# Kernel tuning notes

Hardware: AMD Instinct MI355X
Metric: run time of the kernel (lower is better)

Reference implementation:

```python
import jax, jax.numpy as jnp
import numpy as np

B, T, C, H, W = 32, 128, 64, 8, 8
NF = 64
CIN = C * H * W           # 4096
GOUT = NF * H * W         # 4096


def setup_inputs() -> dict:
    key = jax.random.key(0)
    ks = jax.random.split(key, 9)
    s_in = 1.0 / np.sqrt(CIN)
    return {
        "input1": jax.random.normal(ks[0], (B, T, C, H, W), jnp.float32),
        "input2": jax.random.normal(ks[1], (B, T, C, H, W), jnp.float32),
        "act_weights": jax.random.uniform(ks[2], (3,), jnp.float32),
        "w1": jax.random.normal(ks[3], (NF, CIN), jnp.float32) * s_in,
        "b1": jax.random.normal(ks[4], (NF,), jnp.float32) * s_in,
        "w2": jax.random.normal(ks[5], (NF, CIN), jnp.float32) * s_in,
        "b2": jax.random.normal(ks[6], (NF,), jnp.float32) * s_in,
        "wg": jax.random.normal(ks[7], (GOUT, CIN), jnp.float32) * s_in,
        "bg": jax.random.normal(ks[8], (GOUT,), jnp.float32) * s_in,
    }


def reference(input1, input2, act_weights, w1, b1, w2, b2, wg, bg):
    # flatten spatial+channel dims: [B, T, CIN]
    x1 = input1.reshape(B, T, CIN)
    x2 = input2.reshape(B, T, CIN)
    # 1x1 Conv1d == per-timestep linear projection (computed ONCE, unlike torch src)
    q = jnp.einsum("btc,fc->btf", x1, w1) + b1          # [B, T, NF]
    k = jnp.einsum("btc,fc->btf", x2, w2) + b2          # [B, T, NF]
    g = jnp.einsum("btc,gc->btg", x1, wg) + bg          # [B, T, GOUT]
    # QK^T: conv1(x1)^T @ conv2(x2) -> [B, T, T]
    scores = jnp.einsum("btf,bsf->bts", q, k)
    # three activation branches fused via weighted sum; softmax dim=1 (over first T axis)
    act = (act_weights[0] * jax.nn.relu(scores)
           + act_weights[1] * jax.nn.sigmoid(scores)
           + act_weights[2] * jax.nn.softmax(scores, axis=1))
    out = jnp.einsum("bts,bsg->btg", act, g)            # [B, T, GOUT]
    return out.reshape(B, T, NF, H, W)
```

## Files before the change

### kernel.cpp

```cpp
#include <hip/hip_runtime.h>
#include <math.h>

#define B_   32
#define T_   128
#define CIN  4096
#define NF   64
#define GOUT 4096

typedef unsigned short u16;
typedef __attribute__((ext_vector_type(4))) float  f32x4;
typedef __attribute__((ext_vector_type(8))) __bf16 bf16x8;
typedef __attribute__((ext_vector_type(8))) u16    u16x8;

__device__ __forceinline__ u16 f2bf(float f) {
  union { float f; unsigned u; } v; v.f = f;
  unsigned r = v.u + 0x7fffu + ((v.u >> 16) & 1u);
  return (u16)(r >> 16);
}

__device__ __forceinline__ void gload_lds16(const void* g, void* l) {
  __builtin_amdgcn_global_load_lds(
      (const __attribute__((address_space(1))) void*)g,
      (__attribute__((address_space(3))) void*)l, 16, 0, 0);
}

__global__ void k_conv_wg(const float* __restrict__ wg, u16* __restrict__ wgb) {
  size_t i = ((size_t)blockIdx.x * 256 + threadIdx.x) * 8;
  f32x4 a = *(const f32x4*)&wg[i];
  f32x4 b = *(const f32x4*)&wg[i + 4];
  u16x8 o;
  o[0]=f2bf(a[0]); o[1]=f2bf(a[1]); o[2]=f2bf(a[2]); o[3]=f2bf(a[3]);
  o[4]=f2bf(b[0]); o[5]=f2bf(b[1]); o[6]=f2bf(b[2]); o[7]=f2bf(b[3]);
  *(u16x8*)&wgb[i] = o;
}

__global__ __launch_bounds__(256) void k_x1t(const float* __restrict__ x1,
                                             u16* __restrict__ x1tb) {
  __shared__ float tile[128][132];
  const int b = blockIdx.y, c0 = blockIdx.x * 128, tid = threadIdx.x;
  #pragma unroll
  for (int i = 0; i < 16; ++i) {
    int f = tid + i * 256; int s = f >> 5, c4 = (f & 31) * 4;
    f32x4 v = *(const f32x4*)&x1[((size_t)b * 128 + s) * CIN + c0 + c4];
    tile[s][c4] = v[0]; tile[s][c4+1] = v[1]; tile[s][c4+2] = v[2]; tile[s][c4+3] = v[3];
  }
  __syncthreads();
  const int c = tid >> 1, sh = (tid & 1) * 64;
  #pragma unroll
  for (int i = 0; i < 8; ++i) {
    u16x8 o;
    #pragma unroll
    for (int j = 0; j < 8; ++j) o[j] = f2bf(tile[sh + i * 8 + j][c]);
    *(u16x8*)&x1tb[((size_t)b * CIN + c0 + c) * 128 + sh + i * 8] = o;
  }
}

__global__ __launch_bounds__(256) void k_qk_partial(
    const float* __restrict__ x1, const float* __restrict__ x2,
    const float* __restrict__ w1, const float* __restrict__ w2,
    float* __restrict__ part) {
  const int rt = blockIdx.x, ksp = blockIdx.y, which = blockIdx.z;
  const float* __restrict__ X = which ? x2 : x1;
  const float* __restrict__ W = which ? w2 : w1;
  __shared__ __align__(16) u16 Xs[128 * 64];
  __shared__ __align__(16) u16 Ws[64 * 64];
  const int tid = threadIdx.x;
  const int wave = tid >> 6, lane = tid & 63;
  const int fr = lane & 15, fk = lane >> 4;
  f32x4 acc[2][4];
  #pragma unroll
  for (int a = 0; a < 2; ++a)
    #pragma unroll
    for (int b = 0; b < 4; ++b) acc[a][b] = (f32x4){0.f, 0.f, 0.f, 0.f};

  for (int step = 0; step < 8; ++step) {
    const int kbase = ksp * 512 + step * 64;
    __syncthreads();
    #pragma unroll
    for (int i = 0; i < 4; ++i) {
      int ci = tid + i * 256; int r = ci >> 3, c8 = ci & 7;
      const float* s = &X[((size_t)rt * 128 + r) * CIN + kbase + c8 * 8];
      f32x4 va = *(const f32x4*)s, vb = *(const f32x4*)(s + 4);
      bf16x8 o;
      o[0]=(__bf16)va[0]; o[1]=(__bf16)va[1]; o[2]=(__bf16)va[2]; o[3]=(__bf16)va[3];
      o[4]=(__bf16)vb[0]; o[5]=(__bf16)vb[1]; o[6]=(__bf16)vb[2]; o[7]=(__bf16)vb[3];
      *(bf16x8*)((char*)Xs + r * 128 + ((c8 ^ (r & 7)) * 16)) = o;
    }
    #pragma unroll
    for (int i = 0; i < 2; ++i) {
      int ci = tid + i * 256; int r = ci >> 3, c8 = ci & 7;
      const float* s = &W[(size_t)r * CIN + kbase + c8 * 8];
      f32x4 va = *(const f32x4*)s, vb = *(const f32x4*)(s + 4);
      bf16x8 o;
      o[0]=(__bf16)va[0]; o[1]=(__bf16)va[1]; o[2]=(__bf16)va[2]; o[3]=(__bf16)va[3];
      o[4]=(__bf16)vb[0]; o[5]=(__bf16)vb[1]; o[6]=(__bf16)vb[2]; o[7]=(__bf16)vb[3];
      *(bf16x8*)((char*)Ws + r * 128 + ((c8 ^ (r & 7)) * 16)) = o;
    }
    __syncthreads();
    #pragma unroll
    for (int ks = 0; ks < 2; ++ks) {
      bf16x8 af[2], bf[4];
      #pragma unroll
      for (int a = 0; a < 2; ++a) {
        int ra = wave * 32 + a * 16 + fr;
        af[a] = *(const bf16x8*)((const char*)Xs + ra * 128 + (((ks * 4 + fk) ^ (ra & 7)) * 16));
      }
      #pragma unroll
      for (int b = 0; b < 4; ++b) {
        int rb = b * 16 + fr;
        bf[b] = *(const bf16x8*)((const char*)Ws + rb * 128 + (((ks * 4 + fk) ^ (rb & 7)) * 16));
      }
      #pragma unroll
      for (int a = 0; a < 2; ++a)
        #pragma unroll
        for (int b = 0; b < 4; ++b)
          acc[a][b] = __builtin_amdgcn_mfma_f32_16x16x32_bf16(af[a], bf[b], acc[a][b], 0, 0, 0);
    }
  }
  float* dst = part + ((size_t)(which * 8 + ksp)) * 262144;
  #pragma unroll
  for (int a = 0; a < 2; ++a)
    #pragma unroll
    for (int j = 0; j < 4; ++j) {
      int row = rt * 128 + wave * 32 + a * 16 + fk * 4 + j;
      #pragma unroll
      for (int b = 0; b < 4; ++b)
        dst[(size_t)row * 64 + b * 16 + fr] = acc[a][b][j];
    }
}

__global__ void k_qk_reduce(const float* __restrict__ part,
                            const float* __restrict__ b1, const float* __restrict__ b2,
                            float* __restrict__ q, float* __restrict__ kq) {
  int idx = blockIdx.x * 256 + threadIdx.x;
  int which = idx >> 18;
  int rn = idx & 262143;
  int n = rn & 63;
  float s = which ? b2[n] : b1[n];
  const float* p = part + (size_t)which * 8 * 262144 + rn;
  #pragma unroll
  for (int i = 0; i < 8; ++i) s += p[(size_t)i * 262144];
  (which ? kq : q)[rn] = s;
}

__global__ void k_scores(const float* __restrict__ q, const float* __restrict__ kbuf,
                         const float* __restrict__ aw,
                         u16* __restrict__ actb, float* __restrict__ rowsum) {
  __shared__ float qs[128][66], ks2[128][66];
  __shared__ float sc[128][129];
  __shared__ float mxh[2][128], smh[2][128], rsh[2][128];
  const int b = blockIdx.x, tid = threadIdx.x;
  #pragma unroll
  for (int i = 0; i < 8; ++i) {
    int f = tid + i * 256; int r = f >> 4, c = (f & 15) * 4;
    f32x4 vq = *(const f32x4*)&q[((size_t)b * 128 + r) * 64 + c];
    qs[r][c] = vq[0]; qs[r][c+1] = vq[1]; qs[r][c+2] = vq[2]; qs[r][c+3] = vq[3];
    f32x4 vk = *(const f32x4*)&kbuf[((size_t)b * 128 + r) * 64 + c];
    ks2[r][c] = vk[0]; ks2[r][c+1] = vk[1]; ks2[r][c+2] = vk[2]; ks2[r][c+3] = vk[3];
  }
  __syncthreads();
  const int tx = tid & 15, ty = tid >> 4;
  float a8[8][8] = {};
  for (int c = 0; c < 64; ++c) {
    float qv[8], kv[8];
    #pragma unroll
    for (int i = 0; i < 8; ++i) qv[i] = qs[ty * 8 + i][c];
    #pragma unroll
    for (int j = 0; j < 8; ++j) kv[j] = ks2[tx + j * 16][c];
    #pragma unroll
    for (int i = 0; i < 8; ++i)
      #pragma unroll
      for (int j = 0; j < 8; ++j)
        a8[i][j] += qv[i] * kv[j];
  }
  #pragma unroll
  for (int i = 0; i < 8; ++i)
    #pragma unroll
    for (int j = 0; j < 8; ++j)
      sc[ty * 8 + i][tx + j * 16] = a8[i][j];
  __syncthreads();
  const int sc_ = tid & 127, hh = tid >> 7;
  {
    float m = -INFINITY;
    for (int t = hh * 64; t < hh * 64 + 64; ++t) m = fmaxf(m, sc[t][sc_]);
    mxh[hh][sc_] = m;
  }
  __syncthreads();
  {
    float m = fmaxf(mxh[0][sc_], mxh[1][sc_]);
    float ss = 0.f;
    for (int t = hh * 64; t < hh * 64 + 64; ++t) ss += __expf(sc[t][sc_] - m);
    smh[hh][sc_] = ss;
  }
  __syncthreads();
  const float w0 = aw[0], w1a = aw[1], w2a = aw[2];
  #pragma unroll
  for (int i = 0; i < 8; ++i)
    #pragma unroll
    for (int j = 0; j < 8; ++j) {
      int t = ty * 8 + i, s = tx + j * 16;
      float m = fmaxf(mxh[0][s], mxh[1][s]);
      float dn = smh[0][s] + smh[1][s];
      float v = sc[t][s];
      float av = w0 * fmaxf(v, 0.f)
               + w1a * (1.f / (1.f + __expf(-v)))
               + w2a * (__expf(v - m) / dn);
      actb[((size_t)b * 128 + t) * 128 + s] = f2bf(av);
      sc[t][s] = av;
    }
  __syncthreads();
  {
    int t = tid & 127;
    float s_ = 0.f;
    for (int s = hh * 64; s < hh * 64 + 64; ++s) s_ += sc[t][s];
    rsh[hh][t] = s_;
  }
  __syncthreads();
  if (tid < 128) rowsum[b * 128 + tid] = rsh[0][tid] + rsh[1][tid];
}

__global__ __launch_bounds__(256) void k_y(const u16* __restrict__ actb,
                                           const u16* __restrict__ x1tb,
                                           u16* __restrict__ yb) {
  __shared__ __align__(16) u16 Ab[128 * 128];
  __shared__ __align__(16) u16 Bs[128 * 128];
  const int bb = blockIdx.y, c0 = blockIdx.x * 128, tid = threadIdx.x;
  const int wave = tid >> 6, lane = tid & 63;
  const int wm = wave >> 1, wn = wave & 1;
  const int fr = lane & 15, fk = lane >> 4;
  #pragma unroll
  for (int i = 0; i < 8; ++i) {
    int ci = tid + i * 256; int r = ci >> 4, c16 = ci & 15;
    u16x8 va = *(const u16x8*)&actb[((size_t)bb * 128 + r) * 128 + c16 * 8];
    *(u16x8*)((char*)Ab + r * 256 + ((c16 ^ (r & 15)) * 16)) = va;
    u16x8 vb = *(const u16x8*)&x1tb[((size_t)bb * CIN + c0 + r) * 128 + c16 * 8];
    *(u16x8*)((char*)Bs + r * 256 + ((c16 ^ (r & 15)) * 16)) = vb;
  }
  __syncthreads();
  f32x4 acc[4][4];
  #pragma unroll
  for (int a = 0; a < 4; ++a)
    #pragma unroll
    for (int b = 0; b < 4; ++b) acc[a][b] = (f32x4){0.f, 0.f, 0.f, 0.f};
  #pragma unroll
  for (int ks = 0; ks < 4; ++ks) {
    bf16x8 af[4], bf[4];
    #pragma unroll
    for (int a = 0; a < 4; ++a) {
      int ra = wm * 64 + a * 16 + fr;
      af[a] = *(const bf16x8*)((const char*)Ab + ra * 256 + (((ks * 4 + fk) ^ (ra & 15)) * 16));
    }
    #pragma unroll
    for (int b = 0; b < 4; ++b) {
      int rb = wn * 64 + b * 16 + fr;
      bf[b] = *(const bf16x8*)((const char*)Bs + rb * 256 + (((ks * 4 + fk) ^ (rb & 15)) * 16));
    }
    #pragma unroll
    for (int a = 0; a < 4; ++a)
      #pragma unroll
      for (int b = 0; b < 4; ++b)
        acc[a][b] = __builtin_amdgcn_mfma_f32_16x16x32_bf16(af[a], bf[b], acc[a][b], 0, 0, 0);
  }
  #pragma unroll
  for (int a = 0; a < 4; ++a)
    #pragma unroll
    for (int j = 0; j < 4; ++j) {
      int t = wm * 64 + a * 16 + fk * 4 + j;
      #pragma unroll
      for (int b = 0; b < 4; ++b) {
        int c = c0 + wn * 64 + b * 16 + fr;
        yb[((size_t)bb * 128 + t) * CIN + c] = f2bf(acc[a][b][j]);
      }
    }
}

#define BM 128
#define BN 128
#define BK 64
__global__ __launch_bounds__(256) void k_gemm(
    const u16* __restrict__ A, const u16* __restrict__ Bw,
    const float* __restrict__ rowsum, const float* __restrict__ bg,
    float* __restrict__ C) {
  __shared__ __align__(16) u16 As[BM * BK];
  __shared__ __align__(16) u16 Bs[BN * BK];
  const int tid = threadIdx.x;
  const int wave = tid >> 6, lane = tid & 63;
  const int orig = blockIdx.y * 32 + blockIdx.x;
  const int wgid = (orig & 7) * 128 + (orig >> 3);
  const int row0 = (wgid >> 5) * BM, col0 = (wgid & 31) * BN;
  const int wm = wave >> 1, wn = wave & 1;
  const int fr = lane & 15, fk = lane >> 4;

  const int srow = tid >> 3;
  const int schunk = (tid & 7) ^ (srow & 7);
  const u16* Abase = A + (size_t)(row0 + srow) * CIN + schunk * 8;
  const u16* Bbase = Bw + (size_t)(col0 + srow) * CIN + schunk * 8;

  f32x4 acc[4][4];
  #pragma unroll
  for (int a = 0; a < 4; ++a)
    #pragma unroll
    for (int b = 0; b < 4; ++b) acc[a][b] = (f32x4){0.f, 0.f, 0.f, 0.f};

  for (int kt = 0; kt < CIN; kt += BK) {
    #pragma unroll
    for (int i = 0; i < 4; ++i) {
      gload_lds16(Abase + (size_t)i * 32 * CIN + kt, (char*)As + i * 4096 + wave * 1024);
      gload_lds16(Bbase + (size_t)i * 32 * CIN + kt, (char*)Bs + i * 4096 + wave * 1024);
    }
    __syncthreads();
    #pragma unroll
    for (int ks = 0; ks < 2; ++ks) {
      bf16x8 af[4], bf[4];
      #pragma unroll
      for (int a = 0; a < 4; ++a) {
        int r = wm * 64 + a * 16 + fr;
        int ch = (ks * 4 + fk) ^ (r & 7);
        af[a] = *(const bf16x8*)((const char*)As + r * 128 + ch * 16);
      }
      #pragma unroll
      for (int b = 0; b < 4; ++b) {
        int r = wn * 64 + b * 16 + fr;
        int ch = (ks * 4 + fk) ^ (r & 7);
        bf[b] = *(const bf16x8*)((const char*)Bs + r * 128 + ch * 16);
      }
      #pragma unroll
      for (int a = 0; a < 4; ++a)
        #pragma unroll
        for (int b = 0; b < 4; ++b)
          acc[a][b] = __builtin_amdgcn_mfma_f32_16x16x32_bf16(af[a], bf[b], acc[a][b], 0, 0, 0);
    }
    __syncthreads();
  }

  float bgv[4];
  #pragma unroll
  for (int b = 0; b < 4; ++b) bgv[b] = bg[col0 + wn * 64 + b * 16 + fr];
  #pragma unroll
  for (int a = 0; a < 4; ++a)
    #pragma unroll
    for (int j = 0; j < 4; ++j) {
      int r = row0 + wm * 64 + a * 16 + fk * 4 + j;
      float rs = rowsum[r];
      #pragma unroll
      for (int b = 0; b < 4; ++b) {
        int c = col0 + wn * 64 + b * 16 + fr;
        C[(size_t)r * GOUT + c] = acc[a][b][j] + rs * bgv[b];
      }
    }
}

extern "C" void kernel_launch(void* const* d_in, const int* in_sizes, int n_in,
                              void* d_out, int out_size, void* d_ws, size_t ws_size,
                              hipStream_t stream) {
  const float* x1 = (const float*)d_in[0];
  const float* x2 = (const float*)d_in[1];
  const float* aw = (const float*)d_in[2];
  const float* w1 = (const float*)d_in[3];
  const float* b1 = (const float*)d_in[4];
  const float* w2 = (const float*)d_in[5];
  const float* b2 = (const float*)d_in[6];
  const float* wg = (const float*)d_in[7];
  const float* bg = (const float*)d_in[8];
  float* out = (float*)d_out;
  char* ws = (char*)d_ws;

  float* q    = (float*)(ws);
  float* kq   = (float*)(ws + 1048576);
  u16*   actb = (u16*)(ws + 2097152);
  float* rsum = (float*)(ws + 3145728);
  u16*   wgb  = (u16*)(ws + 4194304);
  u16*   x1tb = (u16*)(ws + 37748736);
  u16*   yb   = (u16*)(ws + 71303168);
  float* part = (float*)(ws + 71303168);

  hipLaunchKernelGGL(k_conv_wg,    dim3(8192),      dim3(256), 0, stream, wg, wgb);
  hipLaunchKernelGGL(k_x1t,        dim3(32, 32),    dim3(256), 0, stream, x1, x1tb);
  hipLaunchKernelGGL(k_qk_partial, dim3(32, 8, 2),  dim3(256), 0, stream,
                     x1, x2, w1, w2, part);
  hipLaunchKernelGGL(k_qk_reduce,  dim3(2048),      dim3(256), 0, stream, part, b1, b2, q, kq);
  hipLaunchKernelGGL(k_scores,     dim3(32),        dim3(256), 0, stream, q, kq, aw, actb, rsum);
  hipLaunchKernelGGL(k_y,          dim3(32, 32),    dim3(256), 0, stream, actb, x1tb, yb);
  hipLaunchKernelGGL(k_gemm,       dim3(32, 32),    dim3(256), 0, stream, yb, wgb, rsum, bg, out);
}
```

Before: 449.7 us.

## Split scores kernel across key blocks and pipeline the final GEMM with 256x256 tiles

```diff
diff --git a/kernel.cpp b/kernel.cpp
--- a/kernel.cpp
+++ b/kernel.cpp
@@ -22,6 +22,12 @@
   __builtin_amdgcn_global_load_lds(
       (const __attribute__((address_space(1))) void*)g,
       (__attribute__((address_space(3))) void*)l, 16, 0, 0);
+}
+
+template<int N> __device__ __forceinline__ void waitvm() {
+  if constexpr (N == 8) asm volatile("s_waitcnt vmcnt(8)" ::: "memory");
+  else if constexpr (N == 4) asm volatile("s_waitcnt vmcnt(4)" ::: "memory");
+  else asm volatile("s_waitcnt vmcnt(0)" ::: "memory");
 }
 
 __global__ void k_conv_wg(const float* __restrict__ wg, u16* __restrict__ wgb) {
@@ -143,80 +149,89 @@
   (which ? kq : q)[rn] = s;
 }
 
-__global__ void k_scores(const float* __restrict__ q, const float* __restrict__ kbuf,
-                         const float* __restrict__ aw,
-                         u16* __restrict__ actb, float* __restrict__ rowsum) {
-  __shared__ float qs[128][66], ks2[128][66];
-  __shared__ float sc[128][129];
-  __shared__ float mxh[2][128], smh[2][128], rsh[2][128];
-  const int b = blockIdx.x, tid = threadIdx.x;
+__global__ __launch_bounds__(256) void k_scores(
+    const float* __restrict__ q, const float* __restrict__ kbuf,
+    const float* __restrict__ aw, u16* __restrict__ actb,
+    float* __restrict__ rsum_part) {
+  __shared__ float qs[128][68];
+  __shared__ float ksm[32][76];
+  __shared__ float lred[16][33];
+  __shared__ float colm[32], colsum[32];
+  __shared__ float rsl[128][17];
+  const int b = blockIdx.x, sblk = blockIdx.y, s0 = sblk * 32, tid = threadIdx.x;
+  const int tx = tid & 15, ty = tid >> 4;
   #pragma unroll
   for (int i = 0; i < 8; ++i) {
-    int f = tid + i * 256; int r = f >> 4, c = (f & 15) * 4;
-    f32x4 vq = *(const f32x4*)&q[((size_t)b * 128 + r) * 64 + c];
-    qs[r][c] = vq[0]; qs[r][c+1] = vq[1]; qs[r][c+2] = vq[2]; qs[r][c+3] = vq[3];
-    f32x4 vk = *(const f32x4*)&kbuf[((size_t)b * 128 + r) * 64 + c];
-    ks2[r][c] = vk[0]; ks2[r][c+1] = vk[1]; ks2[r][c+2] = vk[2]; ks2[r][c+3] = vk[3];
-  }
-  __syncthreads();
-  const int tx = tid & 15, ty = tid >> 4;
-  float a8[8][8] = {};
-  for (int c = 0; c < 64; ++c) {
-    float qv[8], kv[8];
-    #pragma unroll
-    for (int i = 0; i < 8; ++i) qv[i] = qs[ty * 8 + i][c];
-    #pragma unroll
-    for (int j = 0; j < 8; ++j) kv[j] = ks2[tx + j * 16][c];
-    #pragma unroll
-    for (int i = 0; i < 8; ++i)
-      #pragma unroll
-      for (int j = 0; j < 8; ++j)
-        a8[i][j] += qv[i] * kv[j];
-  }
-  #pragma unroll
-  for (int i = 0; i < 8; ++i)
-    #pragma unroll
-    for (int j = 0; j < 8; ++j)
-      sc[ty * 8 + i][tx + j * 16] = a8[i][j];
-  __syncthreads();
-  const int sc_ = tid & 127, hh = tid >> 7;
+    int f = tid + i * 256; int r = f >> 4, c4 = (f & 15) * 4;
+    *(f32x4*)&qs[r][c4] = *(const f32x4*)&q[((size_t)b * 128 + r) * 64 + c4];
+  }
+  #pragma unroll
+  for (int i = 0; i < 2; ++i) {
+    int f = tid + i * 256; int r = f >> 4, c4 = (f & 15) * 4;
+    *(f32x4*)&ksm[r][c4] = *(const f32x4*)&kbuf[((size_t)b * 128 + s0 + r) * 64 + c4];
+  }
+  __syncthreads();
+  float a8[8][2] = {};
+  for (int c4 = 0; c4 < 64; c4 += 4) {
+    f32x4 kv0 = *(const f32x4*)&ksm[tx * 2][c4];
+    f32x4 kv1 = *(const f32x4*)&ksm[tx * 2 + 1][c4];
+    #pragma unroll
+    for (int i = 0; i < 8; ++i) {
+      f32x4 qv = *(const f32x4*)&qs[ty * 8 + i][c4];
+      a8[i][0] += qv[0]*kv0[0] + qv[1]*kv0[1] + qv[2]*kv0[2] + qv[3]*kv0[3];
+      a8[i][1] += qv[0]*kv1[0] + qv[1]*kv1[1] + qv[2]*kv1[2] + qv[3]*kv1[3];
+    }
+  }
   {
-    float m = -INFINITY;
-    for (int t = hh * 64; t < hh * 64 + 64; ++t) m = fmaxf(m, sc[t][sc_]);
-    mxh[hh][sc_] = m;
-  }
-  __syncthreads();
+    float m0 = a8[0][0], m1 = a8[0][1];
+    #pragma unroll
+    for (int i = 1; i < 8; ++i) { m0 = fmaxf(m0, a8[i][0]); m1 = fmaxf(m1, a8[i][1]); }
+    lred[ty][tx * 2] = m0; lred[ty][tx * 2 + 1] = m1;
+  }
+  __syncthreads();
+  if (tid < 32) {
+    float m = lred[0][tid];
+    #pragma unroll
+    for (int t = 1; t < 16; ++t) m = fmaxf(m, lred[t][tid]);
+    colm[tid] = m;
+  }
+  __syncthreads();
+  const float m0 = colm[tx * 2], m1 = colm[tx * 2 + 1];
   {
-    float m = fmaxf(mxh[0][sc_], mxh[1][sc_]);
-    float ss = 0.f;
-    for (int t = hh * 64; t < hh * 64 + 64; ++t) ss += __expf(sc[t][sc_] - m);
-    smh[hh][sc_] = ss;
-  }
-  __syncthreads();
+    float e0 = 0.f, e1 = 0.f;
+    #pragma unroll
+    for (int i = 0; i < 8; ++i) { e0 += __expf(a8[i][0] - m0); e1 += __expf(a8[i][1] - m1); }
+    lred[ty][tx * 2] = e0; lred[ty][tx * 2 + 1] = e1;
+  }
+  __syncthreads();
+  if (tid < 32) {
+    float s = 0.f;
+    #pragma unroll
+    for (int t = 0; t < 16; ++t) s += lred[t][tid];
+    colsum[tid] = s;
+  }
+  __syncthreads();
+  const float d0 = colsum[tx * 2], d1 = colsum[tx * 2 + 1];
   const float w0 = aw[0], w1a = aw[1], w2a = aw[2];
   #pragma unroll
-  for (int i = 0; i < 8; ++i)
-    #pragma unroll
-    for (int j = 0; j < 8; ++j) {
-      int t = ty * 8 + i, s = tx + j * 16;
-      float m = fmaxf(mxh[0][s], mxh[1][s]);
-      float dn = smh[0][s] + smh[1][s];
-      float v = sc[t][s];
-      float av = w0 * fmaxf(v, 0.f)
-               + w1a * (1.f / (1.f + __expf(-v)))
-               + w2a * (__expf(v - m) / dn);
-      actb[((size_t)b * 128 + t) * 128 + s] = f2bf(av);
-      sc[t][s] = av;
-    }
-  __syncthreads();
-  {
-    int t = tid & 127;
-    float s_ = 0.f;
-    for (int s = hh * 64; s < hh * 64 + 64; ++s) s_ += sc[t][s];
-    rsh[hh][t] = s_;
-  }
-  __syncthreads();
-  if (tid < 128) rowsum[b * 128 + tid] = rsh[0][tid] + rsh[1][tid];
+  for (int i = 0; i < 8; ++i) {
+    int t = ty * 8 + i;
+    float v0 = a8[i][0], v1 = a8[i][1];
+    float av0 = w0 * fmaxf(v0, 0.f) + w1a * (1.f / (1.f + __expf(-v0)))
+              + w2a * (__expf(v0 - m0) / d0);
+    float av1 = w0 * fmaxf(v1, 0.f) + w1a * (1.f / (1.f + __expf(-v1)))
+              + w2a * (__expf(v1 - m1) / d1);
+    unsigned pk = (unsigned)f2bf(av0) | ((unsigned)f2bf(av1) << 16);
+    *(unsigned*)&actb[((size_t)b * 128 + t) * 128 + s0 + tx * 2] = pk;
+    rsl[t][tx] = av0 + av1;
+  }
+  __syncthreads();
+  if (tid < 128) {
+    float s = 0.f;
+    #pragma unroll
+    for (int x = 0; x < 16; ++x) s += rsl[tid][x];
+    rsum_part[sblk * 4096 + b * 128 + tid] = s;
+  }
 }
 
 __global__ __launch_bounds__(256) void k_y(const u16* __restrict__ actb,
@@ -274,80 +289,121 @@
     }
 }
 
-#define BM 128
-#define BN 128
-#define BK 64
-__global__ __launch_bounds__(256) void k_gemm(
+#define NT 128
+__global__ __launch_bounds__(512, 2) void k_gemm8(
     const u16* __restrict__ A, const u16* __restrict__ Bw,
-    const float* __restrict__ rowsum, const float* __restrict__ bg,
+    const float* __restrict__ rsum_part, const float* __restrict__ bg,
     float* __restrict__ C) {
-  __shared__ __align__(16) u16 As[BM * BK];
-  __shared__ __align__(16) u16 Bs[BN * BK];
+  extern __shared__ __align__(16) char smem[];
   const int tid = threadIdx.x;
   const int wave = tid >> 6, lane = tid & 63;
-  const int orig = blockIdx.y * 32 + blockIdx.x;
-  const int wgid = (orig & 7) * 128 + (orig >> 3);
-  const int row0 = (wgid >> 5) * BM, col0 = (wgid & 31) * BN;
-  const int wm = wave >> 1, wn = wave & 1;
   const int fr = lane & 15, fk = lane >> 4;
-
-  const int srow = tid >> 3;
-  const int schunk = (tid & 7) ^ (srow & 7);
-  const u16* Abase = A + (size_t)(row0 + srow) * CIN + schunk * 8;
-  const u16* Bbase = Bw + (size_t)(col0 + srow) * CIN + schunk * 8;
-
-  f32x4 acc[4][4];
-  #pragma unroll
-  for (int a = 0; a < 4; ++a)
-    #pragma unroll
-    for (int b = 0; b < 4; ++b) acc[a][b] = (f32x4){0.f, 0.f, 0.f, 0.f};
-
-  for (int kt = 0; kt < CIN; kt += BK) {
-    #pragma unroll
-    for (int i = 0; i < 4; ++i) {
-      gload_lds16(Abase + (size_t)i * 32 * CIN + kt, (char*)As + i * 4096 + wave * 1024);
-      gload_lds16(Bbase + (size_t)i * 32 * CIN + kt, (char*)Bs + i * 4096 + wave * 1024);
-    }
-    __syncthreads();
-    #pragma unroll
-    for (int ks = 0; ks < 2; ++ks) {
-      bf16x8 af[4], bf[4];
-      #pragma unroll
-      for (int a = 0; a < 4; ++a) {
-        int r = wm * 64 + a * 16 + fr;
-        int ch = (ks * 4 + fk) ^ (r & 7);
-        af[a] = *(const bf16x8*)((const char*)As + r * 128 + ch * 16);
+  const int wm = wave >> 2, wn = wave & 3;
+  const int bid = blockIdx.x;
+  const int xcd = bid & 7, idx = bid >> 3;
+  const int rowT = (xcd >> 1) * 4 + (idx >> 3);
+  const int colT = (xcd & 1) * 8 + (idx & 7);
+  const int row0 = rowT * 256, col0 = colT * 256;
+
+#define STAGE_UNIT(G, rowstart, isB, u_) do {                                  \
+    char* db_ = smem + ((isB) ? 65536 : 0) + ((u_) & 3) * 16384 + wave * 1024; \
+    _Pragma("unroll")                                                          \
+    for (int l_ = 0; l_ < 2; ++l_) {                                           \
+      int ci_ = l_ * 512 + tid; int p_ = ci_ >> 3, sl_ = ci_ & 7;              \
+      int c_ = sl_ ^ (p_ & 7);                                                 \
+      const u16* src_ = (G) + (size_t)((rowstart) + 2 * p_ + (c_ >> 2)) * CIN  \
+                        + (u_) * 32 + (c_ & 3) * 8;                            \
+      gload_lds16(src_, db_ + l_ * 8192);                                      \
+    }                                                                          \
+  } while (0)
+
+#define LDA_FRAG(dst, q_, rowa) do {                                           \
+    int pA_ = (rowa) >> 1, hA_ = (rowa) & 1;                                   \
+    dst = *(const bf16x8*)(smem + (q_) * 16384 + pA_ * 128                     \
+                           + (((hA_ * 4 + fk) ^ (pA_ & 7)) * 16)); } while (0)
+#define LDB_FRAG(dst, q_, rowb) do {                                           \
+    int pB_ = (rowb) >> 1, hB_ = (rowb) & 1;                                   \
+    dst = *(const bf16x8*)(smem + 65536 + (q_) * 16384 + pB_ * 128             \
+                           + (((hB_ * 4 + fk) ^ (pB_ & 7)) * 16)); } while (0)
+
+  f32x4 acc[8][4];
+  #pragma unroll
+  for (int m = 0; m < 8; ++m)
+    #pragma unroll
+    for (int n = 0; n < 4; ++n) acc[m][n] = (f32x4){0.f, 0.f, 0.f, 0.f};
+
+  STAGE_UNIT(A, row0, 0, 0); STAGE_UNIT(Bw, col0, 1, 0);
+  STAGE_UNIT(A, row0, 0, 1); STAGE_UNIT(Bw, col0, 1, 1);
+  STAGE_UNIT(A, row0, 0, 2); STAGE_UNIT(Bw, col0, 1, 2);
+  waitvm<8>();
+  __builtin_amdgcn_s_barrier();
+  __builtin_amdgcn_sched_barrier(0);
+
+#define SUBTILE(u_, VN_, DOSTG_) do {                                          \
+    const int q_ = (u_) & 3;                                                   \
+    bf16x8 afr[4], bfr[4];                                                     \
+    _Pragma("unroll")                                                          \
+    for (int n = 0; n < 4; ++n) LDB_FRAG(bfr[n], q_, wn * 64 + n * 16 + fr);   \
+    _Pragma("unroll")                                                          \
+    for (int m = 0; m < 4; ++m) LDA_FRAG(afr[m], q_, wm * 128 + m * 16 + fr);  \
+    if (DOSTG_) STAGE_UNIT(A, row0, 0, (u_) + 3);                              \
+    __builtin_amdgcn_s_barrier();                                              \
+    __builtin_amdgcn_sched_barrier(0);                                         \
+    __builtin_amdgcn_s_setprio(1);                                             \
+    _Pragma("unroll")                                                          \
+    for (int m = 0; m < 4; ++m)                                                \
+      _Pragma("unroll")                                                        \
+      for (int n = 0; n < 4; ++n)                                              \
+        acc[m][n] = __builtin_amdgcn_mfma_f32_16x16x32_bf16(afr[m], bfr[n],    \
+                                                            acc[m][n], 0, 0, 0); \
+    __builtin_amdgcn_s_setprio(0);                                             \
+    __builtin_amdgcn_s_barrier();                                              \
+    __builtin_amdgcn_sched_barrier(0);                                         \
+    _Pragma("unroll")                                                          \
+    for (int m = 0; m < 4; ++m)                                                \
+      LDA_FRAG(afr[m], q_, wm * 128 + (m + 4) * 16 + fr);                      \
+    if (DOSTG_) STAGE_UNIT(Bw, col0, 1, (u_) + 3);                             \
+    waitvm<VN_>();                                                             \
+    __builtin_amdgcn_s_barrier();                                              \
+    __builtin_amdgcn_sched_barrier(0);                                         \
+    __builtin_amdgcn_s_setprio(1);                                             \
+    _Pragma("unroll")                                                          \
+    for (int m = 0; m < 4; ++m)                                                \
+      _Pragma("unroll")                                                        \
+      for (int n = 0; n < 4; ++n)                                              \
+        acc[m + 4][n] = __builtin_amdgcn_mfma_f32_16x16x32_bf16(afr[m], bfr[n], \
+                                                            acc[m + 4][n], 0, 0, 0); \
+    __builtin_amdgcn_s_setprio(0);                                             \
+    __builtin_amdgcn_s_barrier();                                              \
+    __builtin_amdgcn_sched_barrier(0);                                         \
+  } while (0)
+
+  #pragma unroll 1
+  for (int u = 0; u < 125; ++u) SUBTILE(u, 8, 1);
+  SUBTILE(125, 4, 0);
+  SUBTILE(126, 0, 0);
+  SUBTILE(127, 0, 0);
+
+  float bgv[4];
+  #pragma unroll
+  for (int n = 0; n < 4; ++n) bgv[n] = bg[col0 + wn * 64 + n * 16 + fr];
+  #pragma unroll
+  for (int m = 0; m < 8; ++m)
+    #pragma unroll
+    for (int j = 0; j < 4; ++j) {
+      int r = row0 + wm * 128 + m * 16 + fk * 4 + j;
+      float rs = rsum_part[r] + rsum_part[4096 + r]
+               + rsum_part[8192 + r] + rsum_part[12288 + r];
+      #pragma unroll
+      for (int n = 0; n < 4; ++n) {
+        int c = col0 + wn * 64 + n * 16 + fr;
+        C[(size_t)r * GOUT + c] = acc[m][n][j] + rs * bgv[n];
       }
-      #pragma unroll
-      for (int b = 0; b < 4; ++b) {
-        int r = wn * 64 + b * 16 + fr;
-        int ch = (ks * 4 + fk) ^ (r & 7);
-        bf[b] = *(const bf16x8*)((const char*)Bs + r * 128 + ch * 16);
-      }
-      #pragma unroll
-      for (int a = 0; a < 4; ++a)
-        #pragma unroll
-        for (int b = 0; b < 4; ++b)
-          acc[a][b] = __builtin_amdgcn_mfma_f32_16x16x32_bf16(af[a], bf[b], acc[a][b], 0, 0, 0);
-    }
-    __syncthreads();
-  }
-
-  float bgv[4];
-  #pragma unroll
-  for (int b = 0; b < 4; ++b) bgv[b] = bg[col0 + wn * 64 + b * 16 + fr];
-  #pragma unroll
-  for (int a = 0; a < 4; ++a)
-    #pragma unroll
-    for (int j = 0; j < 4; ++j) {
-      int r = row0 + wm * 64 + a * 16 + fk * 4 + j;
-      float rs = rowsum[r];
-      #pragma unroll
-      for (int b = 0; b < 4; ++b) {
-        int c = col0 + wn * 64 + b * 16 + fr;
-        C[(size_t)r * GOUT + c] = acc[a][b][j] + rs * bgv[b];
-      }
-    }
+    }
+#undef SUBTILE
+#undef STAGE_UNIT
+#undef LDA_FRAG
+#undef LDB_FRAG
 }
 
 extern "C" void kernel_launch(void* const* d_in, const int* in_sizes, int n_in,
@@ -374,12 +430,16 @@
   u16*   yb   = (u16*)(ws + 71303168);
   float* part = (float*)(ws + 71303168);
 
+  hipFuncSetAttribute((const void*)k_gemm8,
+                      hipFuncAttributeMaxDynamicSharedMemorySize, 131072);
+
   hipLaunchKernelGGL(k_conv_wg,    dim3(8192),      dim3(256), 0, stream, wg, wgb);
   hipLaunchKernelGGL(k_x1t,        dim3(32, 32),    dim3(256), 0, stream, x1, x1tb);
   hipLaunchKernelGGL(k_qk_partial, dim3(32, 8, 2),  dim3(256), 0, stream,
                      x1, x2, w1, w2, part);
   hipLaunchKernelGGL(k_qk_reduce,  dim3(2048),      dim3(256), 0, stream, part, b1, b2, q, kq);
-  hipLaunchKernelGGL(k_scores,     dim3(32),        dim3(256), 0, stream, q, kq, aw, actb, rsum);
+  hipLaunchKernelGGL(k_scores,     dim3(32, 4),     dim3(256), 0, stream, q, kq, aw, actb, rsum);
   hipLaunchKernelGGL(k_y,          dim3(32, 32),    dim3(256), 0, stream, actb, x1tb, yb);
-  hipLaunchKernelGGL(k_gemm,       dim3(32, 32),    dim3(256), 0, stream, yb, wgb, rsum, bg, out);
-}
+  hipLaunchKernelGGL(k_gemm8,      dim3(256),       dim3(512), 131072, stream,
+                     yb, wgb, rsum, bg, out);
+}
```

Measured after the change: 396.0 us. -11.9%, faster.
